# Kernel tuning notes

Hardware: AMD Instinct MI355X
Metric: run time of the kernel (lower is better)

Reference implementation:

```python
import jax, jax.numpy as jnp
import numpy as np

DIM = 1024
NUM_HEADS = 16
HEAD_DIM = DIM // NUM_HEADS
SCALE = HEAD_DIM ** -0.5


def setup_inputs() -> dict:
    key = jax.random.key(0)
    ks = jax.random.split(key, 5)
    B, N, C = 2, 2048, DIM
    x = jax.random.normal(ks[0], (B, N, C), dtype=jnp.float32)
    s = 1.0 / np.sqrt(C)
    W_qkv = jax.random.normal(ks[1], (C, 3 * C), dtype=jnp.float32) * s
    b_qkv = jax.random.normal(ks[2], (3 * C,), dtype=jnp.float32) * 0.01
    W_proj = jax.random.normal(ks[3], (C, C), dtype=jnp.float32) * s
    b_proj = jax.random.normal(ks[4], (C,), dtype=jnp.float32) * 0.01
    return {"x": x, "W_qkv": W_qkv, "b_qkv": b_qkv, "W_proj": W_proj, "b_proj": b_proj}


def reference(x, W_qkv, b_qkv, W_proj, b_proj):
    B, N, C = x.shape
    qkv = x @ W_qkv + b_qkv                      # [B, N, 3C]
    qkv = qkv.reshape(B, N, 3, NUM_HEADS, HEAD_DIM)
    qkv = jnp.transpose(qkv, (2, 0, 3, 1, 4))    # [3, B, H, N, hd]
    # Faithful to source quirk: q = k = v = qkv[2]
    v = qkv[2]
    q = v
    k = v
    attn = jnp.einsum('bhnd,bhmd->bhnm', q, k) * SCALE
    attn = jax.nn.softmax(attn, axis=-1)
    out = jnp.einsum('bhnm,bhmd->bhnd', attn, v)  # [B, H, N, hd]
    out = jnp.transpose(out, (0, 2, 1, 3)).reshape(B, N, C)
    return out @ W_proj + b_proj
```

## Files before the change

kernel.cpp:

```cpp
#include <hip/hip_runtime.h>

typedef __bf16    bf16x4 __attribute__((ext_vector_type(4)));
typedef __bf16    bf16x8 __attribute__((ext_vector_type(8)));
typedef _Float16  f16x2  __attribute__((ext_vector_type(2)));
typedef _Float16  f16x4  __attribute__((ext_vector_type(4)));
typedef _Float16  f16x8  __attribute__((ext_vector_type(8)));
typedef float     f32x4  __attribute__((ext_vector_type(4)));

#define MFMA16x16x32 __builtin_amdgcn_mfma_f32_16x16x32_bf16
#define MFMA16x16x16F __builtin_amdgcn_mfma_f32_16x16x16f16

__device__ __forceinline__ void gload_lds16(const void* g, void* l) {
  __builtin_amdgcn_global_load_lds((const __attribute__((address_space(1))) void*)g,
                                   (__attribute__((address_space(3))) void*)l, 16, 0, 0);
}

__device__ __forceinline__ f16x2 pkrtz(float a, float b) {
  return __builtin_bit_cast(f16x2, __builtin_amdgcn_cvt_pkrtz(a, b));
}

__global__ __launch_bounds__(256) void cvt_f32_bf16(const float* __restrict__ src,
                                                    __bf16* __restrict__ dst, int n4) {
  int i = blockIdx.x * 256 + threadIdx.x;
  if (i >= n4) return;
  const float4 f = ((const float4*)src)[i];
  bf16x4 o;
  o.x = (__bf16)f.x; o.y = (__bf16)f.y; o.z = (__bf16)f.z; o.w = (__bf16)f.w;
  ((bf16x4*)dst)[i] = o;
}

__global__ __launch_bounds__(256) void prep_transpose(const float* __restrict__ Wqkv,
                                                      const float* __restrict__ Wproj,
                                                      __bf16* __restrict__ WvT,
                                                      __bf16* __restrict__ WpT) {
  __shared__ float tile[64][65];
  const float* src; __bf16* dst; int ld, c0;
  if (blockIdx.z == 0) { src = Wqkv; dst = WvT; ld = 3072; c0 = 2048; }
  else                 { src = Wproj; dst = WpT; ld = 1024; c0 = 0; }
  const int k0 = blockIdx.x * 64, n0 = blockIdx.y * 64;
  const int t = threadIdx.x;
#pragma unroll
  for (int i = 0; i < 4; i++) {
    int idx = t + i * 256; int r = idx >> 4, g = idx & 15;
    float4 v = *(const float4*)&src[(size_t)(k0 + r) * ld + c0 + n0 + g * 4];
    tile[r][g * 4 + 0] = v.x; tile[r][g * 4 + 1] = v.y;
    tile[r][g * 4 + 2] = v.z; tile[r][g * 4 + 3] = v.w;
  }
  __syncthreads();
#pragma unroll
  for (int i = 0; i < 4; i++) {
    int idx = t + i * 256; int n = idx >> 4, g = idx & 15;
    bf16x4 o;
    o.x = (__bf16)tile[g * 4 + 0][n]; o.y = (__bf16)tile[g * 4 + 1][n];
    o.z = (__bf16)tile[g * 4 + 2][n]; o.w = (__bf16)tile[g * 4 + 3][n];
    *(bf16x4*)&dst[(size_t)(n0 + n) * 1024 + k0 + g * 4] = o;
  }
}

__global__ __launch_bounds__(256) void build_vt(const __bf16* __restrict__ V,
                                                _Float16* __restrict__ Vt) {
  __shared__ _Float16 tl[64][72];
  const int bh = blockIdx.y, b = bh >> 4, h = bh & 15;
  const int n0 = blockIdx.x * 64;
  const int t = threadIdx.x;
#pragma unroll
  for (int i = 0; i < 2; i++) {
    int idx = t + i * 256; int r = idx >> 3, g = idx & 7;
    bf16x8 v = *(const bf16x8*)&V[(size_t)(b * 2048 + n0 + r) * 1024 + h * 64 + g * 8];
    f16x8 c;
#pragma unroll
    for (int j = 0; j < 8; j++) c[j] = (_Float16)(float)v[j];
    *(f16x8*)&tl[r][g * 8] = c;
  }
  __syncthreads();
#pragma unroll
  for (int i = 0; i < 2; i++) {
    int idx = t + i * 256; int d = idx >> 3, g = idx & 7;
    f16x8 o;
#pragma unroll
    for (int j = 0; j < 8; j++) o[j] = tl[g * 8 + j][d];
    *(f16x8*)&Vt[((size_t)bh * 64 + d) * 2048 + n0 + g * 8] = o;
  }
}

template <bool BF16OUT>
__global__ __launch_bounds__(256) void gemm_bt(const __bf16* __restrict__ A,
                                               const __bf16* __restrict__ Bt,
                                               const float* __restrict__ bias,
                                               void* __restrict__ outp) {
  constexpr int K = 1024, Nn = 1024;
  __shared__ __bf16 lds[2 * 8192];
  const int t = threadIdx.x, w = t >> 6, l = t & 63, lr = l & 15, quad = l >> 4;
  const int m0 = blockIdx.x * 128, n0 = blockIdx.y * 128;
  const int rm = t >> 2, kg = t & 3;

  const __bf16* pA0 = A  + (size_t)(m0 + rm) * K + kg * 8;
  const __bf16* pA1 = pA0 + (size_t)64 * K;
  const __bf16* pB0 = Bt + (size_t)(n0 + rm) * K + kg * 8;
  const __bf16* pB1 = pB0 + (size_t)64 * K;

  f32x4 acc[2][8] = {};

  {
    char* buf = (char*)lds;
    gload_lds16(pA0, buf + t * 16);
    gload_lds16(pA1, buf + t * 16 + 4096);
    gload_lds16(pB0, buf + 8192 + t * 16);
    gload_lds16(pB1, buf + 8192 + t * 16 + 4096);
  }
  for (int it = 0; it < 32; ++it) {
    __syncthreads();
    if (it + 1 < 32) {
      pA0 += 32; pA1 += 32; pB0 += 32; pB1 += 32;
      char* buf = (char*)lds + ((it + 1) & 1) * 16384;
      gload_lds16(pA0, buf + t * 16);
      gload_lds16(pA1, buf + t * 16 + 4096);
      gload_lds16(pB0, buf + 8192 + t * 16);
      gload_lds16(pB1, buf + 8192 + t * 16 + 4096);
    }
    const __bf16* Al = lds + (it & 1) * 8192;
    const __bf16* Bl = Al + 4096;
    bf16x8 af0 = *(const bf16x8*)&Al[(w * 32 + lr) * 32 + quad * 8];
    bf16x8 af1 = *(const bf16x8*)&Al[(w * 32 + 16 + lr) * 32 + quad * 8];
#pragma unroll
    for (int nc = 0; nc < 8; nc++) {
      bf16x8 bv = *(const bf16x8*)&Bl[(nc * 16 + lr) * 32 + quad * 8];
      acc[0][nc] = MFMA16x16x32(af0, bv, acc[0][nc], 0, 0, 0);
      acc[1][nc] = MFMA16x16x32(af1, bv, acc[1][nc], 0, 0, 0);
    }
  }
#pragma unroll
  for (int mr = 0; mr < 2; mr++)
#pragma unroll
    for (int nc = 0; nc < 8; nc++)
#pragma unroll
      for (int r = 0; r < 4; r++) {
        int grow = m0 + w * 32 + mr * 16 + quad * 4 + r;
        int gcol = n0 + nc * 16 + lr;
        float v = acc[mr][nc][r] + bias[gcol];
        if (BF16OUT) ((__bf16*)outp)[(size_t)grow * Nn + gcol] = (__bf16)v;
        else         ((float*)outp)[(size_t)grow * Nn + gcol] = v;
      }
}

__global__ __launch_bounds__(256, 2) void attn_kernel(const __bf16* __restrict__ V,
                                                      const _Float16* __restrict__ Vt,
                                                      __bf16* __restrict__ O) {
  __shared__ char lds[32768];
  const int t = threadIdx.x, w = t >> 6, l = t & 63, lr = l & 15, quad = l >> 4;
  const int bh = blockIdx.y, b = bh >> 4, h = bh & 15;
  const int qb = blockIdx.x * 128 + w * 16;

  const __bf16* Vbh = V + (size_t)b * 2048 * 1024 + h * 64;
  const _Float16* Vtbh = Vt + (size_t)bh * 64 * 2048;

  bf16x8 qf[2][2];
#pragma unroll
  for (int sub = 0; sub < 2; sub++)
#pragma unroll
    for (int ks = 0; ks < 2; ks++)
      qf[sub][ks] = *(const bf16x8*)(Vbh + (size_t)(qb + sub * 64 + lr) * 1024 + ks * 32 + quad * 8);

  const int kva = t >> 3, ua = (t & 7) ^ (kva & 7);
  const int kvb = kva + 32, ub = (t & 7) ^ (kvb & 7);
  const __bf16* pKa = Vbh + (size_t)kva * 1024 + ua * 8;
  const __bf16* pKb = Vbh + (size_t)kvb * 1024 + ub * 8;
  const int kb_ = t >> 7, d_ = (t >> 1) & 63, qh = (t & 1) ^ ((d_ >> 2) & 1);
  const _Float16* pVa = Vtbh + (size_t)d_ * 2048 + kb_ * 16 + qh * 8;
  const _Float16* pVb = pVa + 32;

  const int koff0 = lr * 128 + ((quad ^ (lr & 7)) * 16);
  const int koff1 = lr * 128 + (((4 + quad) ^ (lr & 7)) * 16);
  const int xq = (quad >> 1) ^ ((lr >> 2) & 1);
  const int voff = lr * 32 + xq * 16 + (quad & 1) * 8;

  f32x4 o[2][4] = {};
  f32x4 l5[2] = {};
  f16x4 ones; ones[0] = ones[1] = ones[2] = ones[3] = (_Float16)1.0f;
  const float Cc = 0.18033688011112042f;
  const float C8 = 11.541560327111707f;

  {
    char* Kb = lds; char* Vb = lds + 8192;
    gload_lds16(pKa, Kb + t * 16); gload_lds16(pKb, Kb + t * 16 + 4096);
    gload_lds16(pVa, Vb + t * 16); gload_lds16(pVb, Vb + t * 16 + 4096);
  }
  for (int it = 0; it < 32; ++it) {
    __syncthreads();
    if (it + 1 < 32) {
      pKa += 65536; pKb += 65536; pVa += 64; pVb += 64;
      char* Kb = lds + ((it + 1) & 1) * 16384; char* Vb = Kb + 8192;
      gload_lds16(pKa, Kb + t * 16); gload_lds16(pKb, Kb + t * 16 + 4096);
      gload_lds16(pVa, Vb + t * 16); gload_lds16(pVb, Vb + t * 16 + 4096);
    }
    const char* Kb = lds + (it & 1) * 16384;
    const char* Vb = Kb + 8192;

    f32x4 s[2][4] = {};
#pragma unroll
    for (int ks = 0; ks < 2; ks++) {
      const int ko = ks ? koff1 : koff0;
#pragma unroll
      for (int rb = 0; rb < 4; rb++) {
        bf16x8 kf = *(const bf16x8*)(Kb + ko + rb * 2048);
        s[0][rb] = MFMA16x16x32(kf, qf[0][ks], s[0][rb], 0, 0, 0);
        s[1][rb] = MFMA16x16x32(kf, qf[1][ks], s[1][rb], 0, 0, 0);
      }
    }

    f16x4 pf[2][4];
#pragma unroll
    for (int sub = 0; sub < 2; sub++)
#pragma unroll
      for (int rb = 0; rb < 4; rb++) {
        float p0 = __builtin_amdgcn_exp2f(s[sub][rb][0] * Cc - C8);
        float p1 = __builtin_amdgcn_exp2f(s[sub][rb][1] * Cc - C8);
        float p2 = __builtin_amdgcn_exp2f(s[sub][rb][2] * Cc - C8);
        float p3 = __builtin_amdgcn_exp2f(s[sub][rb][3] * Cc - C8);
        f16x2 lo = pkrtz(p0, p1);
        f16x2 hi = pkrtz(p2, p3);
        pf[sub][rb][0] = lo[0]; pf[sub][rb][1] = lo[1];
        pf[sub][rb][2] = hi[0]; pf[sub][rb][3] = hi[1];
      }

#pragma unroll
    for (int kb = 0; kb < 4; kb++) {
#pragma unroll
      for (int db = 0; db < 4; db++) {
        f16x4 vf = *(const f16x4*)(Vb + voff + db * 512 + kb * 2048);
        o[0][db] = MFMA16x16x16F(pf[0][kb], vf, o[0][db], 0, 0, 0);
        o[1][db] = MFMA16x16x16F(pf[1][kb], vf, o[1][db], 0, 0, 0);
      }
      l5[0] = MFMA16x16x16F(pf[0][kb], ones, l5[0], 0, 0, 0);
      l5[1] = MFMA16x16x16F(pf[1][kb], ones, l5[1], 0, 0, 0);
    }
  }

#pragma unroll
  for (int sub = 0; sub < 2; sub++)
#pragma unroll
    for (int r = 0; r < 4; r++) {
      float lv = 1.0f / l5[sub][r];
      int token = b * 2048 + qb + sub * 64 + quad * 4 + r;
#pragma unroll
      for (int db = 0; db < 4; db++)
        O[(size_t)token * 1024 + h * 64 + db * 16 + lr] = (__bf16)(o[sub][db][r] * lv);
    }
}

extern "C" void kernel_launch(void* const* d_in, const int* in_sizes, int n_in,
                              void* d_out, int out_size, void* d_ws, size_t ws_size,
                              hipStream_t stream) {
  (void)in_sizes; (void)n_in; (void)out_size; (void)ws_size;
  const float* x     = (const float*)d_in[0];
  const float* Wqkv  = (const float*)d_in[1];
  const float* bqkv  = (const float*)d_in[2];
  const float* Wproj = (const float*)d_in[3];
  const float* bproj = (const float*)d_in[4];

  char* ws = (char*)d_ws;
  __bf16*    xb  = (__bf16*)(ws);
  __bf16*    V   = (__bf16*)(ws + (size_t)8  * 1048576);
  _Float16*  Vt  = (_Float16*)(ws + (size_t)16 * 1048576);
  __bf16*    Ob  = (__bf16*)(ws + (size_t)24 * 1048576);
  __bf16*    WvT = (__bf16*)(ws + (size_t)32 * 1048576);
  __bf16*    WpT = (__bf16*)(ws + (size_t)34 * 1048576);

  cvt_f32_bf16<<<4096, 256, 0, stream>>>(x, xb, 1048576);
  prep_transpose<<<dim3(16, 16, 2), 256, 0, stream>>>(Wqkv, Wproj, WvT, WpT);
  gemm_bt<true><<<dim3(32, 8), 256, 0, stream>>>(xb, WvT, bqkv + 2048, V);
  build_vt<<<dim3(32, 32), 256, 0, stream>>>(V, Vt);
  attn_kernel<<<dim3(16, 32), 256, 0, stream>>>(V, Vt, Ob);
  gemm_bt<false><<<dim3(32, 8), 256, 0, stream>>>(Ob, WpT, bproj, d_out);
}
```

Measured before the change: 172.4 us.

## Split attention KV range across two wave groups and shrink GEMM tiles

```diff
diff --git a/kernel.cpp b/kernel.cpp
--- a/kernel.cpp
+++ b/kernel.cpp
@@ -84,72 +84,60 @@
 }
 
 template <bool BF16OUT>
-__global__ __launch_bounds__(256) void gemm_bt(const __bf16* __restrict__ A,
-                                               const __bf16* __restrict__ Bt,
-                                               const float* __restrict__ bias,
-                                               void* __restrict__ outp) {
+__global__ __launch_bounds__(256, 4) void gemm_bt(const __bf16* __restrict__ A,
+                                                  const __bf16* __restrict__ Bt,
+                                                  const float* __restrict__ bias,
+                                                  void* __restrict__ outp) {
   constexpr int K = 1024, Nn = 1024;
-  __shared__ __bf16 lds[2 * 8192];
+  __shared__ __bf16 lds[2 * 4096];
   const int t = threadIdx.x, w = t >> 6, l = t & 63, lr = l & 15, quad = l >> 4;
-  const int m0 = blockIdx.x * 128, n0 = blockIdx.y * 128;
+  const int m0 = blockIdx.x * 64, n0 = blockIdx.y * 64;
   const int rm = t >> 2, kg = t & 3;
 
-  const __bf16* pA0 = A  + (size_t)(m0 + rm) * K + kg * 8;
-  const __bf16* pA1 = pA0 + (size_t)64 * K;
-  const __bf16* pB0 = Bt + (size_t)(n0 + rm) * K + kg * 8;
-  const __bf16* pB1 = pB0 + (size_t)64 * K;
-
-  f32x4 acc[2][8] = {};
-
-  {
-    char* buf = (char*)lds;
-    gload_lds16(pA0, buf + t * 16);
-    gload_lds16(pA1, buf + t * 16 + 4096);
-    gload_lds16(pB0, buf + 8192 + t * 16);
-    gload_lds16(pB1, buf + 8192 + t * 16 + 4096);
-  }
+  const __bf16* pA = A  + (size_t)(m0 + rm) * K + kg * 8;
+  const __bf16* pB = Bt + (size_t)(n0 + rm) * K + kg * 8;
+
+  f32x4 acc[4] = {};
+
+  gload_lds16(pA, (char*)lds + t * 16);
+  gload_lds16(pB, (char*)lds + 4096 + t * 16);
   for (int it = 0; it < 32; ++it) {
     __syncthreads();
     if (it + 1 < 32) {
-      pA0 += 32; pA1 += 32; pB0 += 32; pB1 += 32;
-      char* buf = (char*)lds + ((it + 1) & 1) * 16384;
-      gload_lds16(pA0, buf + t * 16);
-      gload_lds16(pA1, buf + t * 16 + 4096);
-      gload_lds16(pB0, buf + 8192 + t * 16);
-      gload_lds16(pB1, buf + 8192 + t * 16 + 4096);
-    }
-    const __bf16* Al = lds + (it & 1) * 8192;
-    const __bf16* Bl = Al + 4096;
-    bf16x8 af0 = *(const bf16x8*)&Al[(w * 32 + lr) * 32 + quad * 8];
-    bf16x8 af1 = *(const bf16x8*)&Al[(w * 32 + 16 + lr) * 32 + quad * 8];
-#pragma unroll
-    for (int nc = 0; nc < 8; nc++) {
+      pA += 32; pB += 32;
+      char* buf = (char*)lds + ((it + 1) & 1) * 8192;
+      gload_lds16(pA, buf + t * 16);
+      gload_lds16(pB, buf + 4096 + t * 16);
+    }
+    const __bf16* Al = lds + (it & 1) * 4096;
+    const __bf16* Bl = Al + 2048;
+    bf16x8 af = *(const bf16x8*)&Al[(w * 16 + lr) * 32 + quad * 8];
+#pragma unroll
+    for (int nc = 0; nc < 4; nc++) {
       bf16x8 bv = *(const bf16x8*)&Bl[(nc * 16 + lr) * 32 + quad * 8];
-      acc[0][nc] = MFMA16x16x32(af0, bv, acc[0][nc], 0, 0, 0);
-      acc[1][nc] = MFMA16x16x32(af1, bv, acc[1][nc], 0, 0, 0);
-    }
-  }
-#pragma unroll
-  for (int mr = 0; mr < 2; mr++)
-#pragma unroll
-    for (int nc = 0; nc < 8; nc++)
-#pragma unroll
-      for (int r = 0; r < 4; r++) {
-        int grow = m0 + w * 32 + mr * 16 + quad * 4 + r;
-        int gcol = n0 + nc * 16 + lr;
-        float v = acc[mr][nc][r] + bias[gcol];
-        if (BF16OUT) ((__bf16*)outp)[(size_t)grow * Nn + gcol] = (__bf16)v;
-        else         ((float*)outp)[(size_t)grow * Nn + gcol] = v;
-      }
-}
-
-__global__ __launch_bounds__(256, 2) void attn_kernel(const __bf16* __restrict__ V,
+      acc[nc] = MFMA16x16x32(af, bv, acc[nc], 0, 0, 0);
+    }
+  }
+#pragma unroll
+  for (int nc = 0; nc < 4; nc++)
+#pragma unroll
+    for (int r = 0; r < 4; r++) {
+      int grow = m0 + w * 16 + quad * 4 + r;
+      int gcol = n0 + nc * 16 + lr;
+      float v = acc[nc][r] + bias[gcol];
+      if (BF16OUT) ((__bf16*)outp)[(size_t)grow * Nn + gcol] = (__bf16)v;
+      else         ((float*)outp)[(size_t)grow * Nn + gcol] = v;
+    }
+}
+
+__global__ __launch_bounds__(512, 4) void attn_kernel(const __bf16* __restrict__ V,
                                                       const _Float16* __restrict__ Vt,
                                                       __bf16* __restrict__ O) {
-  __shared__ char lds[32768];
+  __shared__ char lds[65536];
   const int t = threadIdx.x, w = t >> 6, l = t & 63, lr = l & 15, quad = l >> 4;
-  const int bh = blockIdx.y, b = bh >> 4, h = bh & 15;
-  const int qb = blockIdx.x * 128 + w * 16;
+  const int bh = blockIdx.x, b = bh >> 4, h = bh & 15;
+  const int qb = blockIdx.y * 128 + (w & 3) * 16;
+  const int part = w >> 2;
 
   const __bf16* Vbh = V + (size_t)b * 2048 * 1024 + h * 64;
   const _Float16* Vtbh = Vt + (size_t)bh * 64 * 2048;
@@ -162,12 +150,11 @@
       qf[sub][ks] = *(const bf16x8*)(Vbh + (size_t)(qb + sub * 64 + lr) * 1024 + ks * 32 + quad * 8);
 
   const int kva = t >> 3, ua = (t & 7) ^ (kva & 7);
-  const int kvb = kva + 32, ub = (t & 7) ^ (kvb & 7);
-  const __bf16* pKa = Vbh + (size_t)kva * 1024 + ua * 8;
-  const __bf16* pKb = Vbh + (size_t)kvb * 1024 + ub * 8;
+  const __bf16* pK0 = Vbh + (size_t)kva * 1024 + ua * 8;
+  const __bf16* pK1 = pK0 + (size_t)64 * 1024;
   const int kb_ = t >> 7, d_ = (t >> 1) & 63, qh = (t & 1) ^ ((d_ >> 2) & 1);
-  const _Float16* pVa = Vtbh + (size_t)d_ * 2048 + kb_ * 16 + qh * 8;
-  const _Float16* pVb = pVa + 32;
+  const _Float16* pV0 = Vtbh + (size_t)d_ * 2048 + kb_ * 16 + qh * 8;
+  const _Float16* pV1 = pV0 + 64;
 
   const int koff0 = lr * 128 + ((quad ^ (lr & 7)) * 16);
   const int koff1 = lr * 128 + (((4 + quad) ^ (lr & 7)) * 16);
@@ -181,19 +168,23 @@
   const float C8 = 11.541560327111707f;
 
   {
-    char* Kb = lds; char* Vb = lds + 8192;
-    gload_lds16(pKa, Kb + t * 16); gload_lds16(pKb, Kb + t * 16 + 4096);
-    gload_lds16(pVa, Vb + t * 16); gload_lds16(pVb, Vb + t * 16 + 4096);
-  }
-  for (int it = 0; it < 32; ++it) {
+    char* base = lds;
+    gload_lds16(pK0, base + t * 16);
+    gload_lds16(pV0, base + 8192 + t * 16);
+    gload_lds16(pK1, base + 16384 + t * 16);
+    gload_lds16(pV1, base + 24576 + t * 16);
+  }
+  for (int it = 0; it < 16; ++it) {
     __syncthreads();
-    if (it + 1 < 32) {
-      pKa += 65536; pKb += 65536; pVa += 64; pVb += 64;
-      char* Kb = lds + ((it + 1) & 1) * 16384; char* Vb = Kb + 8192;
-      gload_lds16(pKa, Kb + t * 16); gload_lds16(pKb, Kb + t * 16 + 4096);
-      gload_lds16(pVa, Vb + t * 16); gload_lds16(pVb, Vb + t * 16 + 4096);
-    }
-    const char* Kb = lds + (it & 1) * 16384;
+    if (it + 1 < 16) {
+      pK0 += 131072; pK1 += 131072; pV0 += 128; pV1 += 128;
+      char* base = lds + ((it + 1) & 1) * 32768;
+      gload_lds16(pK0, base + t * 16);
+      gload_lds16(pV0, base + 8192 + t * 16);
+      gload_lds16(pK1, base + 16384 + t * 16);
+      gload_lds16(pV1, base + 24576 + t * 16);
+    }
+    const char* Kb = lds + (it & 1) * 32768 + part * 16384;
     const char* Vb = Kb + 8192;
 
     f32x4 s[2][4] = {};
@@ -236,16 +227,41 @@
     }
   }
 
-#pragma unroll
-  for (int sub = 0; sub < 2; sub++)
-#pragma unroll
-    for (int r = 0; r < 4; r++) {
-      float lv = 1.0f / l5[sub][r];
-      int token = b * 2048 + qb + sub * 64 + quad * 4 + r;
+  __syncthreads();
+  float* xch = (float*)lds;
+  if (w >= 4) {
+    float* dsto = xch + (w - 4) * 2048;
+#pragma unroll
+    for (int sub = 0; sub < 2; sub++)
 #pragma unroll
       for (int db = 0; db < 4; db++)
-        O[(size_t)token * 1024 + h * 64 + db * 16 + lr] = (__bf16)(o[sub][db][r] * lv);
-    }
+        *(f32x4*)&dsto[(sub * 4 + db) * 256 + l * 4] = o[sub][db];
+    float* dstl = xch + 8192 + (w - 4) * 512;
+    *(f32x4*)&dstl[l * 4] = l5[0];
+    *(f32x4*)&dstl[256 + l * 4] = l5[1];
+  }
+  __syncthreads();
+  if (w < 4) {
+    const float* srco = xch + w * 2048;
+    const float* srcl = xch + 8192 + w * 512;
+#pragma unroll
+    for (int sub = 0; sub < 2; sub++) {
+#pragma unroll
+      for (int db = 0; db < 4; db++)
+        o[sub][db] += *(const f32x4*)&srco[(sub * 4 + db) * 256 + l * 4];
+      l5[sub] += *(const f32x4*)&srcl[sub * 256 + l * 4];
+    }
+#pragma unroll
+    for (int sub = 0; sub < 2; sub++)
+#pragma unroll
+      for (int r = 0; r < 4; r++) {
+        float lv = 1.0f / l5[sub][r];
+        int token = b * 2048 + qb + sub * 64 + quad * 4 + r;
+#pragma unroll
+        for (int db = 0; db < 4; db++)
+          O[(size_t)token * 1024 + h * 64 + db * 16 + lr] = (__bf16)(o[sub][db][r] * lv);
+      }
+  }
 }
 
 extern "C" void kernel_launch(void* const* d_in, const int* in_sizes, int n_in,
@@ -268,8 +284,8 @@
 
   cvt_f32_bf16<<<4096, 256, 0, stream>>>(x, xb, 1048576);
   prep_transpose<<<dim3(16, 16, 2), 256, 0, stream>>>(Wqkv, Wproj, WvT, WpT);
-  gemm_bt<true><<<dim3(32, 8), 256, 0, stream>>>(xb, WvT, bqkv + 2048, V);
+  gemm_bt<true><<<dim3(64, 16), 256, 0, stream>>>(xb, WvT, bqkv + 2048, V);
   build_vt<<<dim3(32, 32), 256, 0, stream>>>(V, Vt);
-  attn_kernel<<<dim3(16, 32), 256, 0, stream>>>(V, Vt, Ob);
-  gemm_bt<false><<<dim3(32, 8), 256, 0, stream>>>(Ob, WpT, bproj, d_out);
-}
+  attn_kernel<<<dim3(32, 16), 512, 0, stream>>>(V, Vt, Ob);
+  gemm_bt<false><<<dim3(64, 16), 256, 0, stream>>>(Ob, WpT, bproj, d_out);
+}
```

Result: faster. 166.7 us (-3.3%).
